# Optimization experiments

Measured on AMD Instinct MI355X. Metric: run time of the kernel, lower is better.

Reference implementation:

```python
import jax, jax.numpy as jnp
import numpy as np

N = 100000       # nodes
E_EDGES = 1000000  # edges
B = 64           # graphs in batch
V_DIM = 128
E_DIM = 16
H = 128
K_HEAD = 4


def _lin(x, w, b):
    return x @ w.T + b


def _gru_cell(x, h, w_ih, b_ih, w_hh, b_hh):
    # torch.nn.GRUCell math
    gi = x @ w_ih.T + b_ih
    gh = h @ w_hh.T + b_hh
    i_r, i_z, i_n = jnp.split(gi, 3, axis=1)
    h_r, h_z, h_n = jnp.split(gh, 3, axis=1)
    r = jax.nn.sigmoid(i_r + h_r)
    z = jax.nn.sigmoid(i_z + h_z)
    n = jnp.tanh(i_n + r * h_n)
    return (1.0 - z) * n + z * h


def _gate(a, b, c, Aw, Ab, Bw, Bb, w_ih, b_ih, w_hh, b_hh):
    # Adaptive_GRU_T
    z = jax.nn.sigmoid(_lin(a, Aw, Ab) + _lin(b, Bw, Bb))
    h = z * b + (1.0 - z) * a
    return _gru_cell(c, h, w_ih, b_ih, w_hh, b_hh)


def _forward(v, e, s, src, dst, graph_id,
             A_w, A_b, B_w, B_b, C_w, C_b, E_w, E_b, K_w, K_b,
             mA_w, mA_b, mB_w, mB_b, mC_w, mC_b, mD_w, mD_b,
             gmA_w, gmA_b, gmB_w, gmB_b, gm_wih, gm_bih, gm_whh, gm_bhh,
             gsA_w, gsA_b, gsB_w, gsB_b, gs_wih, gs_bih, gs_whh, gs_bhh):
    nb = s.shape[0]
    n_nodes = v.shape[0]

    # supernode self-update input
    s2s = jnp.tanh(_lin(s, A_w, A_b))

    # Multi_scale_interaction heads (vectorized over k heads)
    d_node = jnp.tanh(jnp.einsum('nv,khv->nkh', v, mA_w) + mA_b)      # [N,k,H]
    d_sup = jnp.tanh(jnp.einsum('bv,khv->bkh', s, mB_w) + mB_b)       # [B,k,H]
    d_sup_n = d_sup[graph_id]                                          # broadcast_nodes
    a = jnp.einsum('nkh,kh->nk', d_node * d_sup_n, mC_w) + mC_b        # [N,k]
    # per-graph softmax over nodes (dgl.softmax_nodes)
    amax = jax.ops.segment_max(a, graph_id, num_segments=nb)
    aexp = jnp.exp(a - amax[graph_id])
    asum = jax.ops.segment_sum(aexp, graph_id, num_segments=nb)
    attn = aexp / asum[graph_id]                                       # [N,k]
    hD = jnp.einsum('nv,khv->nkh', v, mD_w) + mD_b                     # [N,k,H]
    m2s = jax.ops.segment_sum(hD * attn[:, :, None], graph_id, num_segments=nb)
    m2s = m2s.reshape(nb, -1)                                          # cat over heads
    m2s = jnp.tanh(_lin(m2s, B_w, B_b))

    s2m = jnp.tanh(_lin(s, C_w, C_b))[graph_id]                        # broadcast_nodes

    # edge message: leaky_relu(K(e) * v_src, 0.1), sum-aggregated at dst
    ve = jax.nn.leaky_relu(_lin(e, K_w, K_b) * v[src], negative_slope=0.1)
    sve = jax.ops.segment_sum(ve, dst, num_segments=n_nodes)
    svev = jnp.concatenate([sve, v], axis=1)
    m2m = jax.nn.leaky_relu(_lin(svev, E_w, E_b), negative_slope=0.1)

    update_v = _gate(m2m, s2m, v, gmA_w, gmA_b, gmB_w, gmB_b,
                     gm_wih, gm_bih, gm_whh, gm_bhh)
    update_s = _gate(s2s, m2s, s, gsA_w, gsA_b, gsB_w, gsB_b,
                     gs_wih, gs_bih, gs_whh, gs_bhh)
    return update_v, update_s


def setup_inputs() -> dict:
    key = jax.random.key(0)
    ks = iter(jax.random.split(key, 64))

    def nrm(shape, scale=0.05):
        return jax.random.normal(next(ks), shape, dtype=jnp.float32) * scale

    inp = {}
    inp['v'] = nrm((N, V_DIM), 1.0)
    inp['e'] = nrm((E_EDGES, E_DIM), 1.0)
    inp['s'] = nrm((B, V_DIM), 1.0)
    inp['src'] = jax.random.randint(next(ks), (E_EDGES,), 0, N)
    inp['dst'] = jax.random.randint(next(ks), (E_EDGES,), 0, N)
    inp['graph_id'] = jnp.minimum(jnp.arange(N) // (N // B), B - 1)

    inp['A_w'] = nrm((H, V_DIM)); inp['A_b'] = nrm((H,))
    inp['B_w'] = nrm((H, H * K_HEAD)); inp['B_b'] = nrm((H,))
    inp['C_w'] = nrm((H, V_DIM)); inp['C_b'] = nrm((H,))
    inp['E_w'] = nrm((H, H + V_DIM)); inp['E_b'] = nrm((H,))
    inp['K_w'] = nrm((H, E_DIM)); inp['K_b'] = nrm((H,))

    inp['mA_w'] = nrm((K_HEAD, H, V_DIM)); inp['mA_b'] = nrm((K_HEAD, H))
    inp['mB_w'] = nrm((K_HEAD, H, V_DIM)); inp['mB_b'] = nrm((K_HEAD, H))
    inp['mC_w'] = nrm((K_HEAD, H)); inp['mC_b'] = nrm((K_HEAD,))
    inp['mD_w'] = nrm((K_HEAD, H, V_DIM)); inp['mD_b'] = nrm((K_HEAD, H))

    for p in ('gm', 'gs'):
        inp[p + 'A_w'] = nrm((H, H)); inp[p + 'A_b'] = nrm((H,))
        inp[p + 'B_w'] = nrm((H, H)); inp[p + 'B_b'] = nrm((H,))
        inp[p + '_wih'] = nrm((3 * H, H)); inp[p + '_bih'] = nrm((3 * H,))
        inp[p + '_whh'] = nrm((3 * H, H)); inp[p + '_bhh'] = nrm((3 * H,))
    return inp


def reference(v, e, s, src, dst, graph_id,
              A_w, A_b, B_w, B_b, C_w, C_b, E_w, E_b, K_w, K_b,
              mA_w, mA_b, mB_w, mB_b, mC_w, mC_b, mD_w, mD_b,
              gmA_w, gmA_b, gmB_w, gmB_b, gm_wih, gm_bih, gm_whh, gm_bhh,
              gsA_w, gsA_b, gsB_w, gsB_b, gs_wih, gs_bih, gs_whh, gs_bhh):
    return _forward(v, e, s, src, dst, graph_id,
                    A_w, A_b, B_w, B_b, C_w, C_b, E_w, E_b, K_w, K_b,
                    mA_w, mA_b, mB_w, mB_b, mC_w, mC_b, mD_w, mD_b,
                    gmA_w, gmA_b, gmB_w, gmB_b, gm_wih, gm_bih, gm_whh, gm_bhh,
                    gsA_w, gsA_b, gsB_w, gsB_b, gs_wih, gs_bih, gs_whh, gs_bhh)
```

## Files before the change

### kernel.cpp

```cpp
#include <hip/hip_runtime.h>
#include <math.h>

typedef unsigned int u32;
typedef unsigned short u16;

#define N_NODES 100000
#define N_EDGES 1000000
#define NB      64
#define NODES_PER_G 1562
#define CH64 25

typedef __attribute__((ext_vector_type(8))) short bf16x8;
typedef __attribute__((ext_vector_type(4))) float f32x4;
#define MFMA16 __builtin_amdgcn_mfma_f32_16x16x32_bf16

__device__ __forceinline__ float sigmoidf_(float x){ return 1.f/(1.f+__expf(-x)); }
__device__ __forceinline__ float ftanh(float x){
  float e = __expf(-2.f*fabsf(x));
  float t = (1.f - e)/(1.f + e);
  return copysignf(t, x);
}
__device__ __forceinline__ float bfh(u16 h){ return __uint_as_float(((u32)h)<<16); }

__device__ __forceinline__ float dots(const float* w, const float* x){
  const float4* w4 = (const float4*)w;
  float a = 0.f;
#pragma unroll 8
  for(int i=0;i<32;i++){
    float4 t = w4[i];
    a = fmaf(t.x, x[4*i+0], a);
    a = fmaf(t.y, x[4*i+1], a);
    a = fmaf(t.z, x[4*i+2], a);
    a = fmaf(t.w, x[4*i+3], a);
  }
  return a;
}

__device__ __forceinline__ void cvt2(float a, float b, u32 &hi, u32 &lo){
  u32 ab = __float_as_uint(a), bb = __float_as_uint(b);
  hi = (ab>>16) | (bb & 0xffff0000u);
  float ar = a - __uint_as_float(ab & 0xffff0000u);
  float br = b - __uint_as_float(bb & 0xffff0000u);
  lo = (__float_as_uint(ar)>>16) | (__float_as_uint(br) & 0xffff0000u);
}

__global__ __launch_bounds__(256) void k_prep(const float* __restrict__ ew,
                    const float* __restrict__ ga,
                    const float* __restrict__ wih,
                    const float* __restrict__ whh,
                    const float* __restrict__ maw,
                    u16* __restrict__ hi, u16* __restrict__ lo){
  int i = blockIdx.x*256 + threadIdx.x;
  float x;
  if(i < 32768) x = ew[i];
  else if(i < 49152) x = ga[i-32768];
  else if(i < 147456){
    int rel = i - 49152;
    int jr = rel >> 8, c = rel & 255;
    x = (c < 128) ? whh[jr*128 + c] : wih[jr*128 + (c-128)];
  }
  else if(i < 212992) x = maw[i-147456];
  else return;
  u32 b = __float_as_uint(x);
  u16 h = (u16)(b>>16);
  float hf = __uint_as_float((u32)h<<16);
  float l = x - hf;
  hi[i] = h;
  lo[i] = (u16)(__float_as_uint(l)>>16);
}

__global__ __launch_bounds__(128,4) void k_sup(const float* __restrict__ s,
                      const float* A_w, const float* A_b,
                      const float* C_w, const float* C_b,
                      const float* mB_w, const float* mB_b, const float* mC_w,
                      const float* gmB_w, const float* gmB_b,
                      float* s2s, float* s2m_g, float* w2, float* gmB_lin){
  int b = blockIdx.x, h = threadIdx.x;
  __shared__ float sb[128], s2ml[128];
  sb[h] = s[b*128+h];
  __syncthreads();
  s2s[b*128+h] = ftanh(dots(A_w + h*128, sb) + A_b[h]);
  float sm = ftanh(dots(C_w + h*128, sb) + C_b[h]);
  s2m_g[b*128+h] = sm; s2ml[h] = sm;
  for(int k=0;k<4;k++){
    float d = ftanh(dots(mB_w + (size_t)(k*128+h)*128, sb) + mB_b[k*128+h]);
    w2[b*512 + k*128 + h] = d * mC_w[k*128+h];
  }
  __syncthreads();
  gmB_lin[b*128+h] = dots(gmB_w + h*128, s2ml) + gmB_b[h];
}

__global__ __launch_bounds__(256,3) void k_att(const float* __restrict__ v,
                      const float* __restrict__ w2,
                      const u16* __restrict__ mAhi, const u16* __restrict__ mAlo,
                      const float* __restrict__ mA_b, const float* __restrict__ mC_b,
                      float* __restrict__ asum, float* __restrict__ yg){
  int g = blockIdx.x / CH64, chunk = blockIdx.x % CH64;
  int start = g*NODES_PER_G, end = (g==NB-1)? N_NODES : start+NODES_PER_G;
  int node0 = start + chunk*64;
  int cnt = end - node0; if(cnt<=0) return; if(cnt>64) cnt=64;
  int t = threadIdx.x;
  int lane = t & 63, wv = t>>6;
  int lr = lane & 15, lg = lane >> 4;
  int koff = lg*8;

  __shared__ u16 XH[64][136], XL[64][136];
  __shared__ float ael[64][4];
  __shared__ float yq[4][4][128];
  __shared__ float wl2s[512], bAs[512];

  for(int i=t;i<64*32;i+=256){
    int n=i>>5, c=i&31;
    float4 val = (n<cnt) ? ((const float4*)(v + (size_t)(node0+n)*128))[c]
                         : make_float4(0.f,0.f,0.f,0.f);
    int cc = c<<2;
    u32 h01,l01,h23,l23;
    cvt2(val.x,val.y,h01,l01); cvt2(val.z,val.w,h23,l23);
    *(uint2*)&XH[n][cc] = make_uint2(h01,h23);
    *(uint2*)&XL[n][cc] = make_uint2(l01,l23);
  }
  for(int i=t;i<512;i+=256){ wl2s[i]=w2[g*512+i]; bAs[i]=mA_b[i]; }
  __syncthreads();

  float sr[4][4];
#pragma unroll
  for(int ng=0;ng<4;ng++){
#pragma unroll
    for(int r=0;r<4;r++) sr[ng][r]=0.f;
  }

  for(int tt=0; tt<8; tt++){
    int row = wv*128 + tt*16 + lr;
    const u16* bh  = mAhi + (size_t)row*128 + koff;
    const u16* bl_ = mAlo + (size_t)row*128 + koff;
    bf16x8 wh[4], wl[4];
#pragma unroll
    for(int ks=0;ks<4;ks++){
      wh[ks] = *(const bf16x8*)(bh  + ks*32);
      wl[ks] = *(const bf16x8*)(bl_ + ks*32);
    }
    float bb = bAs[row], ww = wl2s[row];
#pragma unroll
    for(int ng=0;ng<4;ng++){
      const u16* pah = &XH[ng*16+lr][koff];
      const u16* pal = &XL[ng*16+lr][koff];
      f32x4 acc = {0.f,0.f,0.f,0.f};
#pragma unroll
      for(int ks=0;ks<4;ks++){
        bf16x8 ah = *(const bf16x8*)(pah + ks*32);
        bf16x8 al = *(const bf16x8*)(pal + ks*32);
        acc = MFMA16(ah, wh[ks], acc, 0,0,0);
        acc = MFMA16(ah, wl[ks], acc, 0,0,0);
        acc = MFMA16(al, wh[ks], acc, 0,0,0);
      }
#pragma unroll
      for(int r=0;r<4;r++) sr[ng][r] += ftanh(acc[r]+bb)*ww;
    }
  }
#pragma unroll
  for(int ng=0;ng<4;ng++){
#pragma unroll
    for(int m=1;m<16;m<<=1){
      sr[ng][0] += __shfl_xor(sr[ng][0], m, 64);
      sr[ng][1] += __shfl_xor(sr[ng][1], m, 64);
      sr[ng][2] += __shfl_xor(sr[ng][2], m, 64);
      sr[ng][3] += __shfl_xor(sr[ng][3], m, 64);
    }
  }
  if(lr==0){
    float cb = mC_b[wv], la = 0.f;
#pragma unroll
    for(int ng=0;ng<4;ng++){
#pragma unroll
      for(int r=0;r<4;r++){
        int n = ng*16 + lg*4 + r;
        float ae = (n<cnt)? __expf(sr[ng][r]+cb) : 0.f;
        ael[n][wv] = ae; la += ae;
      }
    }
    atomicAdd(&asum[g*4+wv], la);
  }
  __syncthreads();

  {
    int q = t>>6, kk = (t>>4)&3, co = t&15;
    float a8[8];
#pragma unroll
    for(int j=0;j<8;j++) a8[j]=0.f;
    for(int n=q*16; n<q*16+16; n++){
      float w = ael[n][kk];
      bf16x8 hh = *(const bf16x8*)&XH[n][co*8];
      bf16x8 ll = *(const bf16x8*)&XL[n][co*8];
#pragma unroll
      for(int j=0;j<8;j++){
        float vv = bfh((u16)hh[j]) + bfh((u16)ll[j]);
        a8[j] = fmaf(w, vv, a8[j]);
      }
    }
#pragma unroll
    for(int j=0;j<8;j++) yq[q][kk][co*8+j] = a8[j];
  }
  __syncthreads();
  {
    int c = t&127, k0 = t>>7;
#pragma unroll
    for(int jj=0;jj<2;jj++){
      int k = k0 + jj*2;
      float y = yq[0][k][c]+yq[1][k][c]+yq[2][k][c]+yq[3][k][c];
      atomicAdd(&yg[(size_t)g*512 + k*128 + c], y);
    }
  }
}

__global__ __launch_bounds__(256) void k_hist(const int* __restrict__ dst, u32* __restrict__ cnt){
  for(int i = blockIdx.x*256 + threadIdx.x; i < N_EDGES; i += 256*1024){
    int d = dst[i];
    if((u32)d < (u32)N_NODES) atomicAdd(&cnt[d], 1u);
  }
}

__global__ __launch_bounds__(1024) void k_scanA(const u32* __restrict__ cnt,
                        u32* __restrict__ offs, u32* __restrict__ tsum){
  __shared__ u32 wsum[16];
  int b = blockIdx.x, t = threadIdx.x, lane = t&63, w = t>>6;
  int i = b*1024 + t;
  u32 x = (i<N_NODES)? cnt[i] : 0u;
  u32 vsc = x;
#pragma unroll
  for(int o=1;o<64;o<<=1){ u32 y=__shfl_up(vsc,o,64); if(lane>=o) vsc+=y; }
  if(lane==63) wsum[w]=vsc;
  __syncthreads();
  if(w==0 && lane<16){
    u32 s = wsum[lane];
#pragma unroll
    for(int o=1;o<16;o<<=1){ u32 y=__shfl_up(s,o,64); if(lane>=o) s+=y; }
    wsum[lane]=s;
  }
  __syncthreads();
  u32 excl = (w>0 ? wsum[w-1] : 0u) + vsc - x;
  if(i<N_NODES) offs[i]=excl;
  if(t==1023) tsum[b] = wsum[15];
}

__global__ __launch_bounds__(1024) void k_scanB(const u32* __restrict__ tsum,
                        u32* __restrict__ offs, u32* __restrict__ cursor, int nb){
  __shared__ u32 base;
  int b = blockIdx.x, t = threadIdx.x;
  if(t==0){ u32 s=0; for(int j=0;j<b;j++) s+=tsum[j]; base=s; }
  __syncthreads();
  int i = b*1024 + t;
  if(i<N_NODES){ u32 o = offs[i]+base; offs[i]=o; cursor[i]=o; }
  if(b==nb-1 && t==0) offs[N_NODES] = base + tsum[b];
}

__global__ __launch_bounds__(256) void k_fill(const int* __restrict__ src, const int* __restrict__ dst,
                      u32* __restrict__ cursor, uint2* __restrict__ slots){
  for(int i = blockIdx.x*256 + threadIdx.x; i < N_EDGES; i += 256*1024){
    int d = dst[i];
    if((u32)d >= (u32)N_NODES) continue;
    int sj = src[i]; if((u32)sj >= (u32)N_NODES) sj = 0;
    u32 pos = atomicAdd(&cursor[d], 1u);
    slots[pos] = make_uint2((u32)sj, (u32)i);
  }
}

__global__ __launch_bounds__(128,8) void k_gath(const float* __restrict__ v,
                       const float* __restrict__ e,
                       const u32* __restrict__ offs, const uint2* __restrict__ slots,
                       const float* __restrict__ K_w, const float* __restrict__ K_b,
                       float* __restrict__ nbuf){
  int d = blockIdx.x;
  int h = threadIdx.x;
  u32 lo = offs[d], hi = offs[d+1];
  float4 kw0,kw1,kw2,kw3;
  { const float4* q=(const float4*)(K_w + h*16); kw0=q[0]; kw1=q[1]; kw2=q[2]; kw3=q[3]; }
  float kb = K_b[h];
  float acc = 0.f;
  __shared__ float el[16][16];
  __shared__ u32 ssrc[16];
  __shared__ u32 seid[16];
  for(u32 base=lo; base<hi; base+=16){
    int chunk = (int)(hi-base); if(chunk>16) chunk=16;
    if(h<chunk){ uint2 sd = slots[base+h]; ssrc[h]=sd.x; seid[h]=sd.y; }
    __syncthreads();
    for(int i=h; i<chunk*16; i+=128){ int j=i>>4, c=i&15; el[j][c] = e[(size_t)seid[j]*16 + c]; }
    __syncthreads();
    for(int j=0;j<chunk;j++){
      float kv = kb;
      kv=fmaf(kw0.x,el[j][0],kv);  kv=fmaf(kw0.y,el[j][1],kv);
      kv=fmaf(kw0.z,el[j][2],kv);  kv=fmaf(kw0.w,el[j][3],kv);
      kv=fmaf(kw1.x,el[j][4],kv);  kv=fmaf(kw1.y,el[j][5],kv);
      kv=fmaf(kw1.z,el[j][6],kv);  kv=fmaf(kw1.w,el[j][7],kv);
      kv=fmaf(kw2.x,el[j][8],kv);  kv=fmaf(kw2.y,el[j][9],kv);
      kv=fmaf(kw2.z,el[j][10],kv); kv=fmaf(kw2.w,el[j][11],kv);
      kv=fmaf(kw3.x,el[j][12],kv); kv=fmaf(kw3.y,el[j][13],kv);
      kv=fmaf(kw3.z,el[j][14],kv); kv=fmaf(kw3.w,el[j][15],kv);
      float vs = v[(size_t)ssrc[j]*128 + h];
      float val = kv*vs; val = (val>0.f)? val : 0.1f*val;
      acc += val;
    }
    __syncthreads();
  }
  nbuf[(size_t)d*128 + h] = acc;
}

__global__ __launch_bounds__(128,4) void k_edge(const float* __restrict__ v, const float* __restrict__ e,
                       const int* __restrict__ src, const int* __restrict__ dst,
                       const float* K_w, const float* K_b,
                       float* __restrict__ nbuf, int lo, int hi){
  int h = threadIdx.x;
  int e0 = blockIdx.x * 16;
  __shared__ float el[16][16];
  __shared__ int sl[16], dl[16];
  for(int i=h;i<256;i+=128){ int ee=i>>4, c=i&15; el[ee][c]=e[(size_t)(e0+ee)*16+c]; }
  if(h<16){ sl[h]=src[e0+h]; dl[h]=dst[e0+h]; }
  float4 kw[4];
  { const float4* q=(const float4*)(K_w + h*16);
    kw[0]=q[0]; kw[1]=q[1]; kw[2]=q[2]; kw[3]=q[3]; }
  float kb = K_b[h];
  __syncthreads();
  for(int j=0;j<16;j++){
    int dj = dl[j];
    if(dj < lo || dj >= hi) continue;
    int sj = sl[j]; if((u32)sj >= (u32)N_NODES) sj = 0;
    float kv=kb;
#pragma unroll
    for(int i=0;i<4;i++){
      float4 t = kw[i];
      kv = fmaf(t.x, el[j][4*i+0], kv);
      kv = fmaf(t.y, el[j][4*i+1], kv);
      kv = fmaf(t.z, el[j][4*i+2], kv);
      kv = fmaf(t.w, el[j][4*i+3], kv);
    }
    float vs = v[(size_t)sj*128+h];
    float val = kv*vs; val = (val>0.f)? val : 0.1f*val;
    atomicAdd(&nbuf[(size_t)(dj-lo)*128+h], val);
  }
}

__global__ __launch_bounds__(512,4) void k_node(
    const float* __restrict__ v, const int* __restrict__ graph_id,
    const u16* __restrict__ whi, const u16* __restrict__ wlo,
    const float* __restrict__ E_b, const float* __restrict__ gmA_b,
    const float* __restrict__ gmB_lin, const float* __restrict__ s2m_g,
    const float* __restrict__ bih, const float* __restrict__ bhh,
    const float* __restrict__ nbuf, float* __restrict__ out, int lo_, int lim){
  int t = threadIdx.x;
  int nl0 = blockIdx.x*64;
  int node0 = lo_ + nl0;
  int cnt = lim - nl0; if(cnt > 64) cnt = 64;
  int lane = t & 63, wv = t>>6;
  int lr = lane & 15, lg = lane >> 4;
  int koff = lg*8;
  int hh = wv*16 + lr;

  __shared__ u16 XH[64][264];
  __shared__ u16 XL[64][264];
  __shared__ int gid[64];

  for(int i=t; i<64*64; i+=512){
    int n = i>>6, c4 = i&63;
    float4 val;
    if(n < cnt){
      val = (c4<32) ? ((const float4*)(nbuf + (size_t)(nl0+n)*128))[c4]
                    : ((const float4*)(v + (size_t)(node0+n)*128))[c4-32];
    } else val = make_float4(0.f,0.f,0.f,0.f);
    int c = c4<<2;
    u32 h01,l01,h23,l23;
    cvt2(val.x, val.y, h01, l01);
    cvt2(val.z, val.w, h23, l23);
    *(uint2*)&XH[n][c] = make_uint2(h01, h23);
    *(uint2*)&XL[n][c] = make_uint2(l01, l23);
  }
  if(t<64) gid[t] = (t<cnt) ? (graph_id[node0+t] & 63) : 0;
  __syncthreads();

  f32x4 m2m[4];
  {
    f32x4 acc[4];
#pragma unroll
    for(int ng=0;ng<4;ng++){ f32x4 z={0.f,0.f,0.f,0.f}; acc[ng]=z; }
    const u16* bh = whi + (size_t)hh*256 + koff;
    const u16* bl = wlo + (size_t)hh*256 + koff;
#pragma unroll
    for(int ks=0; ks<8; ks++){
      bf16x8 wh_ = *(const bf16x8*)(bh + ks*32);
      bf16x8 wl_ = *(const bf16x8*)(bl + ks*32);
#pragma unroll
      for(int ng=0;ng<4;ng++){
        bf16x8 ah = *(const bf16x8*)&XH[ng*16+lr][koff + ks*32];
        bf16x8 al = *(const bf16x8*)&XL[ng*16+lr][koff + ks*32];
        acc[ng] = MFMA16(ah, wh_, acc[ng], 0,0,0);
        acc[ng] = MFMA16(ah, wl_, acc[ng], 0,0,0);
        acc[ng] = MFMA16(al, wh_, acc[ng], 0,0,0);
      }
    }
    __syncthreads();
    float eb = E_b[hh];
#pragma unroll
    for(int ng=0;ng<4;ng++){
#pragma unroll
      for(int r=0;r<4;r++){
        float m = acc[ng][r] + eb;
        m = (m>0.f)? m : 0.1f*m;
        m2m[ng][r] = m;
        int n = ng*16 + lg*4 + r;
        u32 mb = __float_as_uint(m);
        u16 mh = (u16)(mb>>16);
        XH[n][hh] = mh;
        float mlr = m - __uint_as_float((u32)mh<<16);
        XL[n][hh] = (u16)(__float_as_uint(mlr)>>16);
      }
    }
    __syncthreads();
  }

  {
    f32x4 acc[4];
#pragma unroll
    for(int ng=0;ng<4;ng++){ f32x4 z={0.f,0.f,0.f,0.f}; acc[ng]=z; }
    const u16* bh = whi + 32768 + (size_t)hh*128 + koff;
    const u16* bl = wlo + 32768 + (size_t)hh*128 + koff;
#pragma unroll
    for(int ks=0; ks<4; ks++){
      bf16x8 wh_ = *(const bf16x8*)(bh + ks*32);
      bf16x8 wl_ = *(const bf16x8*)(bl + ks*32);
#pragma unroll
      for(int ng=0;ng<4;ng++){
        bf16x8 ah = *(const bf16x8*)&XH[ng*16+lr][koff + ks*32];
        bf16x8 al = *(const bf16x8*)&XL[ng*16+lr][koff + ks*32];
        acc[ng] = MFMA16(ah, wh_, acc[ng], 0,0,0);
        acc[ng] = MFMA16(ah, wl_, acc[ng], 0,0,0);
        acc[ng] = MFMA16(al, wh_, acc[ng], 0,0,0);
      }
    }
    __syncthreads();
    float ab = gmA_b[hh];
#pragma unroll
    for(int ng=0;ng<4;ng++){
#pragma unroll
      for(int r=0;r<4;r++){
        int n = ng*16 + lg*4 + r;
        int g = gid[n];
        float z = sigmoidf_(acc[ng][r] + ab + gmB_lin[g*128+hh]);
        float hg = z*s2m_g[g*128+hh] + (1.f-z)*m2m[ng][r];
        u32 mb = __float_as_uint(hg);
        u16 mh = (u16)(mb>>16);
        XH[n][hh] = mh;
        float mlr = hg - __uint_as_float((u32)mh<<16);
        XL[n][hh] = (u16)(__float_as_uint(mlr)>>16);
      }
    }
    __syncthreads();
  }

  {
    const u16* wGh = whi + 49152;
    const u16* wGl = wlo + 49152;
    f32x4 rr[4], nn[4];

    {
      f32x4 acc[4];
#pragma unroll
      for(int ng=0;ng<4;ng++){ f32x4 z={0.f,0.f,0.f,0.f}; acc[ng]=z; }
      const u16* ph = wGh + (size_t)hh*256 + koff;
      const u16* pl = wGl + (size_t)hh*256 + koff;
#pragma unroll
      for(int ks=0; ks<8; ks++){
        bf16x8 wh_ = *(const bf16x8*)(ph + ks*32);
        bf16x8 wl_ = *(const bf16x8*)(pl + ks*32);
#pragma unroll
        for(int ng=0;ng<4;ng++){
          bf16x8 ah = *(const bf16x8*)&XH[ng*16+lr][koff + ks*32];
          bf16x8 al = *(const bf16x8*)&XL[ng*16+lr][koff + ks*32];
          acc[ng] = MFMA16(ah, wh_, acc[ng], 0,0,0);
          acc[ng] = MFMA16(ah, wl_, acc[ng], 0,0,0);
          acc[ng] = MFMA16(al, wh_, acc[ng], 0,0,0);
        }
      }
      float bsum = bih[hh] + bhh[hh];
#pragma unroll
      for(int ng=0;ng<4;ng++)
#pragma unroll
        for(int r=0;r<4;r++) rr[ng][r] = sigmoidf_(acc[ng][r] + bsum);
    }

    {
      f32x4 aH[4], aI[4];
#pragma unroll
      for(int ng=0;ng<4;ng++){ f32x4 z={0.f,0.f,0.f,0.f}; aH[ng]=z; aI[ng]=z; }
      const u16* ph = wGh + (size_t)(256+hh)*256 + koff;
      const u16* pl = wGl + (size_t)(256+hh)*256 + koff;
#pragma unroll
      for(int ks=0; ks<4; ks++){
        bf16x8 wh_ = *(const bf16x8*)(ph + ks*32);
        bf16x8 wl_ = *(const bf16x8*)(pl + ks*32);
#pragma unroll
        for(int ng=0;ng<4;ng++){
          bf16x8 ah = *(const bf16x8*)&XH[ng*16+lr][koff + ks*32];
          bf16x8 al = *(const bf16x8*)&XL[ng*16+lr][koff + ks*32];
          aH[ng] = MFMA16(ah, wh_, aH[ng], 0,0,0);
          aH[ng] = MFMA16(ah, wl_, aH[ng], 0,0,0);
          aH[ng] = MFMA16(al, wh_, aH[ng], 0,0,0);
        }
      }
#pragma unroll
      for(int ks=4; ks<8; ks++){
        bf16x8 wh_ = *(const bf16x8*)(ph + ks*32);
        bf16x8 wl_ = *(const bf16x8*)(pl + ks*32);
#pragma unroll
        for(int ng=0;ng<4;ng++){
          bf16x8 ah = *(const bf16x8*)&XH[ng*16+lr][koff + ks*32];
          bf16x8 al = *(const bf16x8*)&XL[ng*16+lr][koff + ks*32];
          aI[ng] = MFMA16(ah, wh_, aI[ng], 0,0,0);
          aI[ng] = MFMA16(ah, wl_, aI[ng], 0,0,0);
          aI[ng] = MFMA16(al, wh_, aI[ng], 0,0,0);
        }
      }
      float bI = bih[256+hh], bH = bhh[256+hh];
#pragma unroll
      for(int ng=0;ng<4;ng++)
#pragma unroll
        for(int r=0;r<4;r++)
          nn[ng][r] = ftanh((aI[ng][r]+bI) + rr[ng][r]*(aH[ng][r]+bH));
    }

    {
      f32x4 acc[4];
#pragma unroll
      for(int ng=0;ng<4;ng++){ f32x4 z={0.f,0.f,0.f,0.f}; acc[ng]=z; }
      const u16* ph = wGh + (size_t)(128+hh)*256 + koff;
      const u16* pl = wGl + (size_t)(128+hh)*256 + koff;
#pragma unroll
      for(int ks=0; ks<8; ks++){
        bf16x8 wh_ = *(const bf16x8*)(ph + ks*32);
        bf16x8 wl_ = *(const bf16x8*)(pl + ks*32);
#pragma unroll
        for(int ng=0;ng<4;ng++){
          bf16x8 ah = *(const bf16x8*)&XH[ng*16+lr][koff + ks*32];
          bf16x8 al = *(const bf16x8*)&XL[ng*16+lr][koff + ks*32];
          acc[ng] = MFMA16(ah, wh_, acc[ng], 0,0,0);
          acc[ng] = MFMA16(ah, wl_, acc[ng], 0,0,0);
          acc[ng] = MFMA16(al, wh_, acc[ng], 0,0,0);
        }
      }
      float bsum = bih[128+hh] + bhh[128+hh];
#pragma unroll
      for(int ng=0;ng<4;ng++){
#pragma unroll
        for(int r=0;r<4;r++){
          float zz = sigmoidf_(acc[ng][r] + bsum);
          int n = ng*16 + lg*4 + r;
          float hgv = bfh(XH[n][hh]) + bfh(XL[n][hh]);
          if(n < cnt)
            out[(size_t)(node0+n)*128 + hh] = (1.f-zz)*nn[ng][r] + zz*hgv;
        }
      }
    }
  }
}

__global__ __launch_bounds__(128,4) void k_sup2(const float* __restrict__ s,
                       const float* __restrict__ yg, const float* __restrict__ asum,
                       const float* __restrict__ s2s,
                       const float* mD_w, const float* mD_b,
                       const float* B_w, const float* B_b,
                       const float* gsA_w, const float* gsA_b,
                       const float* gsB_w, const float* gsB_b,
                       const float* wih, const float* bih, const float* whh, const float* bhh,
                       float* __restrict__ out){
  int b=blockIdx.x, h=threadIdx.x;
  __shared__ float ygl[512], m2si[512], m2sl[128], s2sl[128], sl[128], hgl[128];
  for(int j=0;j<4;j++){ int kh=h+j*128; ygl[kh]=yg[b*512+kh]; }
  s2sl[h]=s2s[b*128+h];
  sl[h]=s[b*128+h];
  __syncthreads();
  for(int j=0;j<4;j++){
    int kh=h+j*128; int k=kh>>7;
    m2si[kh] = dots(mD_w + (size_t)kh*128, &ygl[k*128]) / asum[b*4+k] + mD_b[kh];
  }
  __syncthreads();
  float acc = B_b[h];
  { const float4* q=(const float4*)(B_w + (size_t)h*512);
#pragma unroll 8
    for(int i=0;i<128;i++){
      float4 p=q[i]; int base=i*4;
      acc=fmaf(p.x,m2si[base+0],acc); acc=fmaf(p.y,m2si[base+1],acc);
      acc=fmaf(p.z,m2si[base+2],acc); acc=fmaf(p.w,m2si[base+3],acc);
    }
  }
  float m2sv = ftanh(acc);
  m2sl[h]=m2sv;
  __syncthreads();
  float zacc = dots(gsA_w+(size_t)h*128, s2sl) + gsA_b[h];
  zacc      += dots(gsB_w+(size_t)h*128, m2sl) + gsB_b[h];
  float z = sigmoidf_(zacc);
  float hg = z*m2sl[h] + (1.f-z)*s2sl[h];
  hgl[h]=hg;
  __syncthreads();
  float gi[3], gh[3];
  for(int j=0;j<3;j++){
    gi[j]=dots(wih+(size_t)(h+j*128)*128, sl)+bih[h+j*128];
    gh[j]=dots(whh+(size_t)(h+j*128)*128, hgl)+bhh[h+j*128];
  }
  float r=sigmoidf_(gi[0]+gh[0]), z2=sigmoidf_(gi[1]+gh[1]);
  float nn=ftanh(gi[2]+r*gh[2]);
  out[(size_t)N_NODES*128 + b*128 + h] = (1.f-z2)*nn + z2*hg;
}

extern "C" void kernel_launch(void* const* d_in, const int* in_sizes, int n_in,
                              void* d_out, int out_size, void* d_ws, size_t ws_size,
                              hipStream_t stream){
  const float* v   = (const float*)d_in[0];
  const float* e   = (const float*)d_in[1];
  const float* s   = (const float*)d_in[2];
  const int* src  = (const int*)d_in[3];
  const int* dst  = (const int*)d_in[4];
  const int* graph_id = (const int*)d_in[5];
  const float* A_w=(const float*)d_in[6];  const float* A_b=(const float*)d_in[7];
  const float* B_w=(const float*)d_in[8];  const float* B_b=(const float*)d_in[9];
  const float* C_w=(const float*)d_in[10]; const float* C_b=(const float*)d_in[11];
  const float* E_w=(const float*)d_in[12]; const float* E_b=(const float*)d_in[13];
  const float* K_w=(const float*)d_in[14]; const float* K_b=(const float*)d_in[15];
  const float* mA_w=(const float*)d_in[16]; const float* mA_b=(const float*)d_in[17];
  const float* mB_w=(const float*)d_in[18]; const float* mB_b=(const float*)d_in[19];
  const float* mC_w=(const float*)d_in[20]; const float* mC_b=(const float*)d_in[21];
  const float* mD_w=(const float*)d_in[22]; const float* mD_b=(const float*)d_in[23];
  const float* gmA_w=(const float*)d_in[24]; const float* gmA_b=(const float*)d_in[25];
  const float* gmB_w=(const float*)d_in[26]; const float* gmB_b=(const float*)d_in[27];
  const float* gm_wih=(const float*)d_in[28]; const float* gm_bih=(const float*)d_in[29];
  const float* gm_whh=(const float*)d_in[30]; const float* gm_bhh=(const float*)d_in[31];
  const float* gsA_w=(const float*)d_in[32]; const float* gsA_b=(const float*)d_in[33];
  const float* gsB_w=(const float*)d_in[34]; const float* gsB_b=(const float*)d_in[35];
  const float* gs_wih=(const float*)d_in[36]; const float* gs_bih=(const float*)d_in[37];
  const float* gs_whh=(const float*)d_in[38]; const float* gs_bhh=(const float*)d_in[39];

  float* ws = (float*)d_ws;
  float* asum    = ws;
  float* yg      = asum + 256;
  float* s2s     = yg + 32768;
  float* s2m_g   = s2s + 8192;
  float* gmB_lin = s2m_g + 8192;
  float* w2      = gmB_lin + 8192;
  u16*   whi     = (u16*)(w2 + 32768);
  u16*   wlo     = whi + 212992;
  const size_t small_f = 256 + 32768 + 8192*3 + 32768 + 212992;

  size_t ws_f = ws_size / 4;

  hipMemsetAsync(asum, 0, (256 + 32768) * sizeof(float), stream);

  k_prep<<<832, 256, 0, stream>>>(E_w, gmA_w, gm_wih, gm_whh, mA_w, whi, wlo);
  k_sup <<<NB, 128, 0, stream>>>(s, A_w,A_b, C_w,C_b, mB_w,mB_b,mC_w, gmB_w,gmB_b,
                                 s2s, s2m_g, w2, gmB_lin);
  k_att <<<NB*CH64, 256, 0, stream>>>(v, w2, whi + 147456, wlo + 147456,
                                      mA_b, mC_b, asum, yg);
  k_sup2<<<NB, 128, 0, stream>>>(s, yg, asum, s2s, mD_w, mD_b, B_w,B_b,
                                 gsA_w,gsA_b, gsB_w,gsB_b,
                                 gs_wih,gs_bih, gs_whh,gs_bhh, (float*)d_out);

  const int SCAN_NB = (N_NODES + 1023) / 1024;
  const size_t csr_off = small_f;
  const size_t csr_f   = 100002 + 100002 + 128 + 2000000;
  const size_t need_csr = csr_off + csr_f + (size_t)N_NODES*128;

  if(ws_f >= need_csr){
    u32*   offs   = (u32*)(ws + csr_off);
    u32*   cursor = offs + 100002;
    u32*   tsum   = cursor + 100002;
    uint2* slots  = (uint2*)(tsum + 128);
    float* nbuf   = (float*)(slots + 1000000);
    hipMemsetAsync(cursor, 0, (size_t)N_NODES*sizeof(u32), stream);
    k_hist<<<1024, 256, 0, stream>>>(dst, cursor);
    k_scanA<<<SCAN_NB, 1024, 0, stream>>>(cursor, offs, tsum);
    k_scanB<<<SCAN_NB, 1024, 0, stream>>>(tsum, offs, cursor, SCAN_NB);
    k_fill<<<1024, 256, 0, stream>>>(src, dst, cursor, slots);
    k_gath<<<N_NODES, 128, 0, stream>>>(v, e, offs, slots, K_w, K_b, nbuf);
    k_node<<<(N_NODES+63)/64, 512, 0, stream>>>(v, graph_id, whi, wlo, E_b, gmA_b,
                                                gmB_lin, s2m_g, gm_bih, gm_bhh,
                                                nbuf, (float*)d_out, 0, N_NODES);
  } else {
    float* nbuf = (float*)(wlo + 212992);
    long avail = (ws_f > small_f) ? (long)(ws_f - small_f) : 0;
    long M = (avail / 128) & ~63L;
    if(M > N_NODES) M = N_NODES;
    if(M < 64) M = 64;
    for(long lo = 0; lo < N_NODES; lo += M){
      long cnt = N_NODES - lo; if(cnt > M) cnt = M;
      int ilo = (int)lo, icnt = (int)cnt;
      hipMemsetAsync(nbuf, 0, (size_t)icnt*128*sizeof(float), stream);
      k_edge<<<N_EDGES/16, 128, 0, stream>>>(v, e, src, dst, K_w, K_b, nbuf, ilo, ilo+icnt);
      k_node<<<(icnt+63)/64, 512, 0, stream>>>(v, graph_id, whi, wlo, E_b, gmA_b,
                                               gmB_lin, s2m_g, gm_bih, gm_bhh,
                                               nbuf, (float*)d_out, ilo, icnt);
    }
  }
}
```

Baseline: 922.6 us.

## Fuse attention-score pass into node kernel to reuse staged node features

Removes the separate attention kernel and computes per-head attention logits, exp weights, segment sums and weighted feature sums inside the node-update kernel, which already stages v in shared memory as split bf16. Each 64-node tile handles up to two graphs by finding the graph boundary and using per-graph weights. The aim is to avoid reading v twice and to drop one launch, with k_sup2 moved to the end of the stream. In exchange the node kernel needs more shared memory and registers, and does more atomics into asum and yg per tile.

```diff
diff --git a/kernel.cpp b/kernel.cpp
--- a/kernel.cpp
+++ b/kernel.cpp
@@ -8,7 +8,6 @@
 #define N_EDGES 1000000
 #define NB      64
 #define NODES_PER_G 1562
-#define CH64 25
 
 typedef __attribute__((ext_vector_type(8))) short bf16x8;
 typedef __attribute__((ext_vector_type(4))) float f32x4;
@@ -88,128 +87,6 @@
   }
   __syncthreads();
   gmB_lin[b*128+h] = dots(gmB_w + h*128, s2ml) + gmB_b[h];
-}
-
-__global__ __launch_bounds__(256,3) void k_att(const float* __restrict__ v,
-                      const float* __restrict__ w2,
-                      const u16* __restrict__ mAhi, const u16* __restrict__ mAlo,
-                      const float* __restrict__ mA_b, const float* __restrict__ mC_b,
-                      float* __restrict__ asum, float* __restrict__ yg){
-  int g = blockIdx.x / CH64, chunk = blockIdx.x % CH64;
-  int start = g*NODES_PER_G, end = (g==NB-1)? N_NODES : start+NODES_PER_G;
-  int node0 = start + chunk*64;
-  int cnt = end - node0; if(cnt<=0) return; if(cnt>64) cnt=64;
-  int t = threadIdx.x;
-  int lane = t & 63, wv = t>>6;
-  int lr = lane & 15, lg = lane >> 4;
-  int koff = lg*8;
-
-  __shared__ u16 XH[64][136], XL[64][136];
-  __shared__ float ael[64][4];
-  __shared__ float yq[4][4][128];
-  __shared__ float wl2s[512], bAs[512];
-
-  for(int i=t;i<64*32;i+=256){
-    int n=i>>5, c=i&31;
-    float4 val = (n<cnt) ? ((const float4*)(v + (size_t)(node0+n)*128))[c]
-                         : make_float4(0.f,0.f,0.f,0.f);
-    int cc = c<<2;
-    u32 h01,l01,h23,l23;
-    cvt2(val.x,val.y,h01,l01); cvt2(val.z,val.w,h23,l23);
-    *(uint2*)&XH[n][cc] = make_uint2(h01,h23);
-    *(uint2*)&XL[n][cc] = make_uint2(l01,l23);
-  }
-  for(int i=t;i<512;i+=256){ wl2s[i]=w2[g*512+i]; bAs[i]=mA_b[i]; }
-  __syncthreads();
-
-  float sr[4][4];
-#pragma unroll
-  for(int ng=0;ng<4;ng++){
-#pragma unroll
-    for(int r=0;r<4;r++) sr[ng][r]=0.f;
-  }
-
-  for(int tt=0; tt<8; tt++){
-    int row = wv*128 + tt*16 + lr;
-    const u16* bh  = mAhi + (size_t)row*128 + koff;
-    const u16* bl_ = mAlo + (size_t)row*128 + koff;
-    bf16x8 wh[4], wl[4];
-#pragma unroll
-    for(int ks=0;ks<4;ks++){
-      wh[ks] = *(const bf16x8*)(bh  + ks*32);
-      wl[ks] = *(const bf16x8*)(bl_ + ks*32);
-    }
-    float bb = bAs[row], ww = wl2s[row];
-#pragma unroll
-    for(int ng=0;ng<4;ng++){
-      const u16* pah = &XH[ng*16+lr][koff];
-      const u16* pal = &XL[ng*16+lr][koff];
-      f32x4 acc = {0.f,0.f,0.f,0.f};
-#pragma unroll
-      for(int ks=0;ks<4;ks++){
-        bf16x8 ah = *(const bf16x8*)(pah + ks*32);
-        bf16x8 al = *(const bf16x8*)(pal + ks*32);
-        acc = MFMA16(ah, wh[ks], acc, 0,0,0);
-        acc = MFMA16(ah, wl[ks], acc, 0,0,0);
-        acc = MFMA16(al, wh[ks], acc, 0,0,0);
-      }
-#pragma unroll
-      for(int r=0;r<4;r++) sr[ng][r] += ftanh(acc[r]+bb)*ww;
-    }
-  }
-#pragma unroll
-  for(int ng=0;ng<4;ng++){
-#pragma unroll
-    for(int m=1;m<16;m<<=1){
-      sr[ng][0] += __shfl_xor(sr[ng][0], m, 64);
-      sr[ng][1] += __shfl_xor(sr[ng][1], m, 64);
-      sr[ng][2] += __shfl_xor(sr[ng][2], m, 64);
-      sr[ng][3] += __shfl_xor(sr[ng][3], m, 64);
-    }
-  }
-  if(lr==0){
-    float cb = mC_b[wv], la = 0.f;
-#pragma unroll
-    for(int ng=0;ng<4;ng++){
-#pragma unroll
-      for(int r=0;r<4;r++){
-        int n = ng*16 + lg*4 + r;
-        float ae = (n<cnt)? __expf(sr[ng][r]+cb) : 0.f;
-        ael[n][wv] = ae; la += ae;
-      }
-    }
-    atomicAdd(&asum[g*4+wv], la);
-  }
-  __syncthreads();
-
-  {
-    int q = t>>6, kk = (t>>4)&3, co = t&15;
-    float a8[8];
-#pragma unroll
-    for(int j=0;j<8;j++) a8[j]=0.f;
-    for(int n=q*16; n<q*16+16; n++){
-      float w = ael[n][kk];
-      bf16x8 hh = *(const bf16x8*)&XH[n][co*8];
-      bf16x8 ll = *(const bf16x8*)&XL[n][co*8];
-#pragma unroll
-      for(int j=0;j<8;j++){
-        float vv = bfh((u16)hh[j]) + bfh((u16)ll[j]);
-        a8[j] = fmaf(w, vv, a8[j]);
-      }
-    }
-#pragma unroll
-    for(int j=0;j<8;j++) yq[q][kk][co*8+j] = a8[j];
-  }
-  __syncthreads();
-  {
-    int c = t&127, k0 = t>>7;
-#pragma unroll
-    for(int jj=0;jj<2;jj++){
-      int k = k0 + jj*2;
-      float y = yq[0][k][c]+yq[1][k][c]+yq[2][k][c]+yq[3][k][c];
-      atomicAdd(&yg[(size_t)g*512 + k*128 + c], y);
-    }
-  }
 }
 
 __global__ __launch_bounds__(256) void k_hist(const int* __restrict__ dst, u32* __restrict__ cnt){
@@ -344,6 +221,9 @@
     const float* __restrict__ E_b, const float* __restrict__ gmA_b,
     const float* __restrict__ gmB_lin, const float* __restrict__ s2m_g,
     const float* __restrict__ bih, const float* __restrict__ bhh,
+    const float* __restrict__ w2, const float* __restrict__ mA_b,
+    const float* __restrict__ mC_b,
+    float* __restrict__ asum, float* __restrict__ yg,
     const float* __restrict__ nbuf, float* __restrict__ out, int lo_, int lim){
   int t = threadIdx.x;
   int nl0 = blockIdx.x*64;
@@ -357,6 +237,10 @@
   __shared__ u16 XH[64][264];
   __shared__ u16 XL[64][264];
   __shared__ int gid[64];
+  __shared__ float wl2[2][512];
+  __shared__ float attp[4][2][64];
+  __shared__ float ael[64][4];
+  __shared__ int b0s;
 
   for(int i=t; i<64*64; i+=512){
     int n = i>>6, c4 = i&63;
@@ -372,8 +256,97 @@
     *(uint2*)&XH[n][c] = make_uint2(h01, h23);
     *(uint2*)&XL[n][c] = make_uint2(l01, l23);
   }
-  if(t<64) gid[t] = (t<cnt) ? (graph_id[node0+t] & 63) : 0;
-  __syncthreads();
+  if(t<64) gid[t] = graph_id[node0 + ((t<cnt)? t : (cnt-1))] & 63;
+  if(t==0) b0s = 64;
+  __syncthreads();
+  if(t>0 && t<64 && gid[t]!=gid[t-1]) b0s = t;
+  __syncthreads();
+  int b0 = b0s, gA = gid[0], gB = gid[63];
+  wl2[0][t&511] = w2[gA*512 + (t&511)];
+  wl2[1][t&511] = w2[gB*512 + (t&511)];
+  __syncthreads();
+
+  {
+    int k = wv>>1, half = wv&1;
+    const u16* mAhi = whi + 147456;
+    const u16* mAlo = wlo + 147456;
+    float sr[4][4];
+#pragma unroll
+    for(int ng=0;ng<4;ng++){
+#pragma unroll
+      for(int r=0;r<4;r++) sr[ng][r]=0.f;
+    }
+#pragma unroll
+    for(int tt=0; tt<4; tt++){
+      int row = k*128 + (half*4+tt)*16 + lr;
+      const u16* bh  = mAhi + (size_t)row*128 + koff;
+      const u16* bl_ = mAlo + (size_t)row*128 + koff;
+      bf16x8 wh[4], wl[4];
+#pragma unroll
+      for(int ks=0;ks<4;ks++){
+        wh[ks] = *(const bf16x8*)(bh  + ks*32);
+        wl[ks] = *(const bf16x8*)(bl_ + ks*32);
+      }
+      float bb = mA_b[row];
+      float wA = wl2[0][row & 511], wB = wl2[1][row & 511];
+#pragma unroll
+      for(int ng=0;ng<4;ng++){
+        f32x4 acc = {0.f,0.f,0.f,0.f};
+#pragma unroll
+        for(int ks=0;ks<4;ks++){
+          bf16x8 ah = *(const bf16x8*)&XH[ng*16+lr][128 + koff + ks*32];
+          bf16x8 al = *(const bf16x8*)&XL[ng*16+lr][128 + koff + ks*32];
+          acc = MFMA16(ah, wh[ks], acc, 0,0,0);
+          acc = MFMA16(ah, wl[ks], acc, 0,0,0);
+          acc = MFMA16(al, wh[ks], acc, 0,0,0);
+        }
+#pragma unroll
+        for(int r=0;r<4;r++){
+          int n = ng*16 + lg*4 + r;
+          float ww = (n >= b0) ? wB : wA;
+          sr[ng][r] += ftanh(acc[r]+bb)*ww;
+        }
+      }
+    }
+#pragma unroll
+    for(int ng=0;ng<4;ng++){
+#pragma unroll
+      for(int m=1;m<16;m<<=1){
+        sr[ng][0] += __shfl_xor(sr[ng][0], m, 64);
+        sr[ng][1] += __shfl_xor(sr[ng][1], m, 64);
+        sr[ng][2] += __shfl_xor(sr[ng][2], m, 64);
+        sr[ng][3] += __shfl_xor(sr[ng][3], m, 64);
+      }
+    }
+    if(lr==0){
+#pragma unroll
+      for(int ng=0;ng<4;ng++)
+#pragma unroll
+        for(int r=0;r<4;r++) attp[k][half][ng*16+lg*4+r] = sr[ng][r];
+    }
+    __syncthreads();
+    if(t < 256){
+      int n = t & 63, kk = t >> 6;
+      float ae = 0.f;
+      if(n < cnt){
+        ae = __expf(attp[kk][0][n] + attp[kk][1][n] + mC_b[kk]);
+        atomicAdd(&asum[gid[n]*4 + kk], ae);
+      }
+      ael[n][kk] = ae;
+    }
+    __syncthreads();
+    {
+      int kk = t >> 7, c = t & 127;
+      float yA = 0.f, yB = 0.f;
+      for(int n=0; n<64; n++){
+        float w = ael[n][kk];
+        float vv = bfh(XH[n][128+c]) + bfh(XL[n][128+c]);
+        if(n < b0) yA = fmaf(w, vv, yA); else yB = fmaf(w, vv, yB);
+      }
+      atomicAdd(&yg[(size_t)gA*512 + kk*128 + c], yA);
+      if(b0 < 64) atomicAdd(&yg[(size_t)gB*512 + kk*128 + c], yB);
+    }
+  }
 
   f32x4 m2m[4];
   {
@@ -653,11 +626,6 @@
   k_prep<<<832, 256, 0, stream>>>(E_w, gmA_w, gm_wih, gm_whh, mA_w, whi, wlo);
   k_sup <<<NB, 128, 0, stream>>>(s, A_w,A_b, C_w,C_b, mB_w,mB_b,mC_w, gmB_w,gmB_b,
                                  s2s, s2m_g, w2, gmB_lin);
-  k_att <<<NB*CH64, 256, 0, stream>>>(v, w2, whi + 147456, wlo + 147456,
-                                      mA_b, mC_b, asum, yg);
-  k_sup2<<<NB, 128, 0, stream>>>(s, yg, asum, s2s, mD_w, mD_b, B_w,B_b,
-                                 gsA_w,gsA_b, gsB_w,gsB_b,
-                                 gs_wih,gs_bih, gs_whh,gs_bhh, (float*)d_out);
 
   const int SCAN_NB = (N_NODES + 1023) / 1024;
   const size_t csr_off = small_f;
@@ -678,6 +646,7 @@
     k_gath<<<N_NODES, 128, 0, stream>>>(v, e, offs, slots, K_w, K_b, nbuf);
     k_node<<<(N_NODES+63)/64, 512, 0, stream>>>(v, graph_id, whi, wlo, E_b, gmA_b,
                                                 gmB_lin, s2m_g, gm_bih, gm_bhh,
+                                                w2, mA_b, mC_b, asum, yg,
                                                 nbuf, (float*)d_out, 0, N_NODES);
   } else {
     float* nbuf = (float*)(wlo + 212992);
@@ -692,7 +661,12 @@
       k_edge<<<N_EDGES/16, 128, 0, stream>>>(v, e, src, dst, K_w, K_b, nbuf, ilo, ilo+icnt);
       k_node<<<(icnt+63)/64, 512, 0, stream>>>(v, graph_id, whi, wlo, E_b, gmA_b,
                                                gmB_lin, s2m_g, gm_bih, gm_bhh,
+                                               w2, mA_b, mC_b, asum, yg,
                                                nbuf, (float*)d_out, ilo, icnt);
     }
   }
-}
+
+  k_sup2<<<NB, 128, 0, stream>>>(s, yg, asum, s2s, mD_w, mD_b, B_w,B_b,
+                                 gsA_w,gsA_b, gsB_w,gsB_b,
+                                 gs_wih,gs_bih, gs_whh,gs_bhh, (float*)d_out);
+}
```

New measurement: 2.192 ms. 2.38x slower.

## Double k_att node tile to 128 with 512-thread blocks splitting rows per head

Applied to the files above, without the earlier changes.

The attention-scoring kernel now handles 128 nodes per block with 8 waves. Each head's 128 weight rows are split across two waves, and the partial scores are combined through shared memory before the exp and per-graph sum. This halves the number of times mA weight fragments are reloaded per node and halves the atomics into asum and yg. In exchange it uses more LDS per block, allows fewer blocks (about 832 versus 1600), and adds an extra barrier.

```diff
diff --git a/kernel.cpp b/kernel.cpp
--- a/kernel.cpp
+++ b/kernel.cpp
@@ -8,7 +8,7 @@
 #define N_EDGES 1000000
 #define NB      64
 #define NODES_PER_G 1562
-#define CH64 25
+#define CH128 13
 
 typedef __attribute__((ext_vector_type(8))) short bf16x8;
 typedef __attribute__((ext_vector_type(4))) float f32x4;
@@ -90,26 +90,27 @@
   gmB_lin[b*128+h] = dots(gmB_w + h*128, s2ml) + gmB_b[h];
 }
 
-__global__ __launch_bounds__(256,3) void k_att(const float* __restrict__ v,
+__global__ __launch_bounds__(512,2) void k_att(const float* __restrict__ v,
                       const float* __restrict__ w2,
                       const u16* __restrict__ mAhi, const u16* __restrict__ mAlo,
                       const float* __restrict__ mA_b, const float* __restrict__ mC_b,
                       float* __restrict__ asum, float* __restrict__ yg){
-  int g = blockIdx.x / CH64, chunk = blockIdx.x % CH64;
+  int g = blockIdx.x / CH128, chunk = blockIdx.x % CH128;
   int start = g*NODES_PER_G, end = (g==NB-1)? N_NODES : start+NODES_PER_G;
-  int node0 = start + chunk*64;
-  int cnt = end - node0; if(cnt<=0) return; if(cnt>64) cnt=64;
+  int node0 = start + chunk*128;
+  int cnt = end - node0; if(cnt<=0) return; if(cnt>128) cnt=128;
   int t = threadIdx.x;
   int lane = t & 63, wv = t>>6;
   int lr = lane & 15, lg = lane >> 4;
   int koff = lg*8;
 
-  __shared__ u16 XH[64][136], XL[64][136];
-  __shared__ float ael[64][4];
-  __shared__ float yq[4][4][128];
+  __shared__ u16 XH[128][136], XL[128][136];
+  __shared__ float ael[128][4];
+  __shared__ float attp[4][2][128];
+  __shared__ float yq[8][4][128];
   __shared__ float wl2s[512], bAs[512];
 
-  for(int i=t;i<64*32;i+=256){
+  for(int i=t;i<128*32;i+=512){
     int n=i>>5, c=i&31;
     float4 val = (n<cnt) ? ((const float4*)(v + (size_t)(node0+n)*128))[c]
                          : make_float4(0.f,0.f,0.f,0.f);
@@ -119,18 +120,19 @@
     *(uint2*)&XH[n][cc] = make_uint2(h01,h23);
     *(uint2*)&XL[n][cc] = make_uint2(l01,l23);
   }
-  for(int i=t;i<512;i+=256){ wl2s[i]=w2[g*512+i]; bAs[i]=mA_b[i]; }
-  __syncthreads();
-
-  float sr[4][4];
-#pragma unroll
-  for(int ng=0;ng<4;ng++){
+  { wl2s[t]=w2[g*512+t]; bAs[t]=mA_b[t]; }
+  __syncthreads();
+
+  int k = wv>>1, half = wv&1;
+  float sr[8][4];
+#pragma unroll
+  for(int ng=0;ng<8;ng++){
 #pragma unroll
     for(int r=0;r<4;r++) sr[ng][r]=0.f;
   }
 
-  for(int tt=0; tt<8; tt++){
-    int row = wv*128 + tt*16 + lr;
+  for(int tt=0; tt<4; tt++){
+    int row = k*128 + (half*4+tt)*16 + lr;
     const u16* bh  = mAhi + (size_t)row*128 + koff;
     const u16* bl_ = mAlo + (size_t)row*128 + koff;
     bf16x8 wh[4], wl[4];
@@ -141,7 +143,7 @@
     }
     float bb = bAs[row], ww = wl2s[row];
 #pragma unroll
-    for(int ng=0;ng<4;ng++){
+    for(int ng=0;ng<8;ng++){
       const u16* pah = &XH[ng*16+lr][koff];
       const u16* pal = &XL[ng*16+lr][koff];
       f32x4 acc = {0.f,0.f,0.f,0.f};
@@ -158,7 +160,7 @@
     }
   }
 #pragma unroll
-  for(int ng=0;ng<4;ng++){
+  for(int ng=0;ng<8;ng++){
 #pragma unroll
     for(int m=1;m<16;m<<=1){
       sr[ng][0] += __shfl_xor(sr[ng][0], m, 64);
@@ -168,17 +170,22 @@
     }
   }
   if(lr==0){
-    float cb = mC_b[wv], la = 0.f;
-#pragma unroll
-    for(int ng=0;ng<4;ng++){
-#pragma unroll
-      for(int r=0;r<4;r++){
-        int n = ng*16 + lg*4 + r;
-        float ae = (n<cnt)? __expf(sr[ng][r]+cb) : 0.f;
-        ael[n][wv] = ae; la += ae;
-      }
-    }
-    atomicAdd(&asum[g*4+wv], la);
+#pragma unroll
+    for(int ng=0;ng<8;ng++)
+#pragma unroll
+      for(int r=0;r<4;r++) attp[k][half][ng*16+lg*4+r] = sr[ng][r];
+  }
+  __syncthreads();
+
+  {
+    int n = t & 127, kk = t >> 7;
+    float ae = 0.f;
+    if(n < cnt) ae = __expf(attp[kk][0][n] + attp[kk][1][n] + mC_b[kk]);
+    ael[n][kk] = ae;
+    float s = ae;
+#pragma unroll
+    for(int o=32;o>0;o>>=1) s += __shfl_xor(s, o, 64);
+    if(lane==0) atomicAdd(&asum[g*4+kk], s);
   }
   __syncthreads();
 
@@ -202,13 +209,11 @@
   }
   __syncthreads();
   {
-    int c = t&127, k0 = t>>7;
-#pragma unroll
-    for(int jj=0;jj<2;jj++){
-      int k = k0 + jj*2;
-      float y = yq[0][k][c]+yq[1][k][c]+yq[2][k][c]+yq[3][k][c];
-      atomicAdd(&yg[(size_t)g*512 + k*128 + c], y);
-    }
+    int c = t&127, kk = t>>7;
+    float y = 0.f;
+#pragma unroll
+    for(int q=0;q<8;q++) y += yq[q][kk][c];
+    atomicAdd(&yg[(size_t)g*512 + kk*128 + c], y);
   }
 }
 
@@ -653,8 +658,8 @@
   k_prep<<<832, 256, 0, stream>>>(E_w, gmA_w, gm_wih, gm_whh, mA_w, whi, wlo);
   k_sup <<<NB, 128, 0, stream>>>(s, A_w,A_b, C_w,C_b, mB_w,mB_b,mC_w, gmB_w,gmB_b,
                                  s2s, s2m_g, w2, gmB_lin);
-  k_att <<<NB*CH64, 256, 0, stream>>>(v, w2, whi + 147456, wlo + 147456,
-                                      mA_b, mC_b, asum, yg);
+  k_att <<<NB*CH128, 512, 0, stream>>>(v, w2, whi + 147456, wlo + 147456,
+                                       mA_b, mC_b, asum, yg);
   k_sup2<<<NB, 128, 0, stream>>>(s, yg, asum, s2s, mD_w, mD_b, B_w,B_b,
                                  gsA_w,gsA_b, gsB_w,gsB_b,
                                  gs_wih,gs_bih, gs_whh,gs_bhh, (float*)d_out);
```

Result: slower. 968.1 us (+4.9%).
